# Kernel optimization log

Measured on AMD Instinct MI355X. Metric: run time of the kernel, lower is better.

## Reference

```python
import jax, jax.numpy as jnp
import numpy as np

B, L, D, NC, H = 2, 192, 768, 4, 256  # batch, seq_len, bert_hidden, num_case(+coref), hidden


def setup_inputs() -> dict:
    key = jax.random.key(0)
    ks = jax.random.split(key, 9)
    s = 0.02  # init scale
    return {
        "sequence_output": jax.random.normal(ks[0], (B, L, D), dtype=jnp.float32),
        "base_score": jax.random.normal(ks[1], (B, L, NC, L), dtype=jnp.float32),
        "Wp": jax.random.normal(ks[2], (D, H), dtype=jnp.float32) * s,
        "bp": jnp.zeros((H,), dtype=jnp.float32),
        "Wa": jax.random.normal(ks[3], (D, NC * H), dtype=jnp.float32) * s,
        "ba": jnp.zeros((NC * H,), dtype=jnp.float32),
        "Wmid": jax.random.normal(ks[4], (NC, H + NC, H), dtype=jnp.float32) * s,
        "bmid": jnp.zeros((NC, H), dtype=jnp.float32),
        "Wout": jax.random.normal(ks[5], (NC, H), dtype=jnp.float32) * s,
    }


def reference(sequence_output, base_score, Wp, bp, Wa, ba, Wmid, bmid, Wout):
    b, l, d = sequence_output.shape
    nc = Wmid.shape[0]
    h = Wp.shape[1]
    # dropout is identity in eval mode
    h_p = sequence_output @ Wp + bp                       # [B, L, H] (predicate)
    h_a = (sequence_output @ Wa + ba).reshape(b, l, nc, h)  # [B, L, NC, H] (argument)
    # broadcast add: predicate axis p, argument axis a -> [B, P, A, NC, H]
    h_pa = jnp.tanh(h_p[:, :, None, None, :] + h_a[:, None, :, :, :])
    # base_score [B, L, NC, L] -> transpose(2,3) -> [B, P, A, NC], expand over case axis
    bs = jnp.swapaxes(base_score, 2, 3)                   # [B, P, A, NC]
    bs = jnp.broadcast_to(bs[:, :, :, None, :], (b, l, l, nc, nc))
    hcat = jnp.concatenate([h_pa, bs], axis=-1)           # [B, P, A, NC, H+NC]
    # per-case mid Linear, batched as a single einsum over the case axis n
    h_mid = jnp.tanh(jnp.einsum('bpanc,nch->bpanh', hcat, Wmid) + bmid)
    out = jnp.einsum('bpanh,nh->bpan', h_mid, Wout)       # [B, P, A, NC]
    return jnp.transpose(out, (0, 1, 3, 2))               # [B, P, NC, A]
```

## Files before the change

kernel.cpp:

```cpp
#include <hip/hip_runtime.h>

#define LSEQ 192
#define DIM  768
#define NCASE 4
#define HID  256
#define BATCH 2

#define TANH_K 2.885390081777927f

typedef float  floatx4 __attribute__((ext_vector_type(4)));
typedef __bf16 bf16x8  __attribute__((ext_vector_type(8)));
typedef __bf16 bf16x4  __attribute__((ext_vector_type(4)));

__device__ __forceinline__ float tanh_pre(float x) {
    float e = __builtin_amdgcn_exp2f(x);
    return 1.0f - 2.0f * __builtin_amdgcn_rcpf(e + 1.0f);
}

__device__ __forceinline__ float tanh_add(float tu, float tv) {
    float den = __builtin_fmaf(tu, tv, 1.0f);
    return (tu + tv) * __builtin_amdgcn_rcpf(den);
}

__device__ __forceinline__ void barrier_lds_only() {
    __builtin_amdgcn_sched_barrier(0);
    __builtin_amdgcn_s_waitcnt(0xC07F);
    __builtin_amdgcn_s_barrier();
    __builtin_amdgcn_sched_barrier(0);
}

template <int CTRL>
__device__ __forceinline__ float dpp_add(float v) {
    int x = __builtin_amdgcn_update_dpp(0, __builtin_bit_cast(int, v),
                                        CTRL, 0xF, 0xF, true);
    return v + __builtin_bit_cast(float, x);
}
__device__ __forceinline__ float row16_reduce(float v) {
    v = dpp_add<0xB1>(v);
    v = dpp_add<0x4E>(v);
    v = dpp_add<0x141>(v);
    v = dpp_add<0x140>(v);
    return v;
}


__global__ __launch_bounds__(256) void prep(
    const float* __restrict__ seq, const float* __restrict__ Wp,
    const float* __restrict__ Wa,  const float* __restrict__ bp,
    const float* __restrict__ ba,  const float* __restrict__ Wmid,
    const float* __restrict__ bmid,
    float* __restrict__ lin, bf16x8* __restrict__ Bpack)
{
    const int blk = blockIdx.x;
    const int tid = threadIdx.x;

    if (blk >= 1920) {
        int u = (blk - 1920) * 256 + tid;
        int lane = u & 63, f = u >> 6;
        int ct = f & 15, nk = f >> 4;
        int kc = nk % 9, n = nk / 9;
        int h = ct * 16 + (lane & 15);
        int kbase = kc * 32 + ((lane >> 4) & 3) * 8;
        bf16x8 v;
        #pragma unroll
        for (int j = 0; j < 8; j++) {
            int k = kbase + j;
            float x;
            if (k < 260)       x = Wmid[(size_t)(n * 260 + k) * 256 + h];
            else if (k == 260) x = bmid[n * 256 + h];
            else               x = 0.0f;
            v[j] = (__bf16)(TANH_K * x);
        }
        Bpack[u] = v;
        return;
    }

    const int w = tid >> 6, lane = tid & 63;
    const int rt = blk / 80, cg = blk % 80;
    const int quad  = lane >> 4;
    const int col16 = lane & 15;

    __shared__ float cmb[3][256];

    const int arow = rt * 16 + col16;
    const int col  = cg * 16 + col16;
    const int kofs = w * 192;
    const float* aptr = seq + (size_t)arow * DIM + kofs + quad * 8;
    const float* wbase = (cg < 16) ? (Wp + col) : (Wa + (col - 256));
    const int    wstr  = (cg < 16) ? HID : (NCASE * HID);

    floatx4 acc = {};
    floatx4 a0 = *(const floatx4*)(aptr);
    floatx4 a1 = *(const floatx4*)(aptr + 4);
    float bv[8];
    #pragma unroll
    for (int j = 0; j < 8; j++)
        bv[j] = wbase[(size_t)(kofs + quad * 8 + j) * wstr];

    #pragma unroll
    for (int kc = 0; kc < 6; kc++) {
        bf16x8 ah, al, bh, bl;
        #pragma unroll
        for (int j = 0; j < 4; j++) {
            __bf16 h0 = (__bf16)a0[j];
            ah[j] = h0; al[j] = (__bf16)(a0[j] - (float)h0);
            __bf16 h1 = (__bf16)a1[j];
            ah[4 + j] = h1; al[4 + j] = (__bf16)(a1[j] - (float)h1);
        }
        #pragma unroll
        for (int j = 0; j < 8; j++) {
            __bf16 h = (__bf16)bv[j];
            bh[j] = h; bl[j] = (__bf16)(bv[j] - (float)h);
        }
        if (kc < 5) {
            a0 = *(const floatx4*)(aptr + (kc + 1) * 32);
            a1 = *(const floatx4*)(aptr + (kc + 1) * 32 + 4);
            #pragma unroll
            for (int j = 0; j < 8; j++)
                bv[j] = wbase[(size_t)(kofs + (kc + 1) * 32 + quad * 8 + j) * wstr];
        }
        acc = __builtin_amdgcn_mfma_f32_16x16x32_bf16(ah, bh, acc, 0, 0, 0);
        acc = __builtin_amdgcn_mfma_f32_16x16x32_bf16(al, bh, acc, 0, 0, 0);
        acc = __builtin_amdgcn_mfma_f32_16x16x32_bf16(ah, bl, acc, 0, 0, 0);
    }

    if (w > 0) *(floatx4*)&cmb[w - 1][lane * 4] = acc;
    __syncthreads();
    if (w == 0) {
        #pragma unroll
        for (int i = 0; i < 3; i++) {
            floatx4 p = *(const floatx4*)&cmb[i][lane * 4];
            acc += p;
        }
        const float bias = (cg < 16) ? bp[col] : ba[col - 256];
        #pragma unroll
        for (int reg = 0; reg < 4; reg++)
            lin[(size_t)(rt * 16 + quad * 4 + reg) * 1280 + col] =
                tanh_pre(TANH_K * (acc[reg] + bias));
    }
}

__global__ __launch_bounds__(512, 6) void refine_main(
    const float* __restrict__ lin,
    const float* __restrict__ base_score,
    const float* __restrict__ Wout,
    const bf16x8* __restrict__ Bpack,
    float* __restrict__ out)
{
    const int bx = blockIdx.x;
    const int n  = blockIdx.y;
    const int b  = blockIdx.z;
    const int ptile = bx / 24, atile = bx % 24;
    const int p0 = ptile * 8, a0r = atile * 8;

    const int tid   = threadIdx.x;
    const int w     = tid >> 6;
    const int lane  = tid & 63;
    const int quad  = lane >> 4;
    const int col16 = lane & 15;

    __shared__ __align__(16) __bf16 A0[256 * 8];
    __shared__ __align__(16) __bf16 A1[256 * 8];
    __shared__ float red[8][64];

    const int s_g    = tid >> 1;
    const int h2     = tid & 1;
    const int l_g    = s_g & 63;
    const int m_gen  = ((s_g >> 6) << 4) + (l_g & 15);
    const int kq     = (l_g >> 4) * 8 + h2 * 4;
    const int quad_g = l_g >> 4;

    const int pg = p0 + (m_gen >> 3), ag = a0r + (m_gen & 7);
    const float* hp_ptr = lin + (size_t)(b * LSEQ + pg) * 1280 + kq;
    const float* ha_ptr = lin + (size_t)(b * LSEQ + ag) * 1280 + 256 + n * 256 + kq;

    const bf16x8* bbase = Bpack + ((size_t)(n * 9) * 16 + w * 2) * 64 + lane;

    float bs4[4] = {};
    if (quad_g == 0 && h2 == 0) {
        #pragma unroll
        for (int j = 0; j < 4; j++)
            bs4[j] = base_score[((size_t)(b * LSEQ + pg) * NCASE + j) * LSEQ + ag];
    }
    float wo[2];
    #pragma unroll
    for (int ct = 0; ct < 2; ct++)
        wo[ct] = Wout[n * 256 + w * 32 + ct * 16 + col16];

    bf16x8 bcur[2];
    #pragma unroll
    for (int ct = 0; ct < 2; ct++) bcur[ct] = bbase[ct * 64];

    floatx4 hp = *(const floatx4*)(hp_ptr);
    floatx4 ha = *(const floatx4*)(ha_ptr);
    {
        bf16x4 av;
        #pragma unroll
        for (int j = 0; j < 4; j++) av[j] = (__bf16)tanh_add(hp[j], ha[j]);
        *(bf16x4*)&A0[tid * 4] = av;
    }
    hp = *(const floatx4*)(hp_ptr + 32);
    ha = *(const floatx4*)(ha_ptr + 32);
    barrier_lds_only();

    floatx4 acc[4][2] = {};

    #pragma unroll
    for (int kc = 0; kc < 9; kc++) {
        bf16x8 bnext[2];
        if (kc < 8) {
            #pragma unroll
            for (int ct = 0; ct < 2; ct++)
                bnext[ct] = bbase[((kc + 1) * 16 + ct) * 64];
        }
        if (kc < 7) {
            floatx4 u0 = hp, v0 = ha;
            if (kc < 6) {
                hp = *(const floatx4*)(hp_ptr + (kc + 2) * 32);
                ha = *(const floatx4*)(ha_ptr + (kc + 2) * 32);
            }
            bf16x4 av;
            #pragma unroll
            for (int j = 0; j < 4; j++) av[j] = (__bf16)tanh_add(u0[j], v0[j]);
            __bf16* buf = ((kc + 1) & 1) ? A1 : A0;
            *(bf16x4*)&buf[tid * 4] = av;
        } else if (kc == 7) {
            bf16x4 av = {};
            if (quad_g == 0) {
                if (h2 == 0) {
                    #pragma unroll
                    for (int j = 0; j < 4; j++) av[j] = (__bf16)bs4[j];
                } else {
                    av[0] = (__bf16)1.0f;
                }
            }
            *(bf16x4*)&A0[tid * 4] = av;
        }

        const __bf16* rb = (kc & 1) ? A1 : A0;
        bf16x8 af[4];
        #pragma unroll
        for (int rt = 0; rt < 4; rt++)
            af[rt] = *(const bf16x8*)&rb[(rt * 64 + lane) * 8];
        #pragma unroll
        for (int rt = 0; rt < 4; rt++)
            #pragma unroll
            for (int ct = 0; ct < 2; ct++)
                acc[rt][ct] = __builtin_amdgcn_mfma_f32_16x16x32_bf16(
                    af[rt], bcur[ct], acc[rt][ct], 0, 0, 0);
        #pragma unroll
        for (int ct = 0; ct < 2; ct++) bcur[ct] = bnext[ct];
        if (kc < 8) barrier_lds_only();
    }

    #pragma unroll
    for (int rt = 0; rt < 4; rt++) {
        #pragma unroll
        for (int reg = 0; reg < 4; reg++) {
            float rs = tanh_pre(acc[rt][0][reg]) * wo[0]
                     + tanh_pre(acc[rt][1][reg]) * wo[1];
            rs = row16_reduce(rs);
            if (col16 == 0) red[w][rt * 16 + quad * 4 + reg] = rs;
        }
    }
    barrier_lds_only();

    if (tid < 64) {
        float total = red[0][tid] + red[1][tid] + red[2][tid] + red[3][tid]
                    + red[4][tid] + red[5][tid] + red[6][tid] + red[7][tid];
        const int p = p0 + (tid >> 3), a = a0r + (tid & 7);
        out[((size_t)(b * LSEQ + p) * NCASE + n) * LSEQ + a] = total;
    }
}

extern "C" void kernel_launch(void* const* d_in, const int* in_sizes, int n_in,
                              void* d_out, int out_size, void* d_ws, size_t ws_size,
                              hipStream_t stream) {
    const float* seq  = (const float*)d_in[0];
    const float* bsc  = (const float*)d_in[1];
    const float* Wp   = (const float*)d_in[2];
    const float* bp   = (const float*)d_in[3];
    const float* Wa   = (const float*)d_in[4];
    const float* ba   = (const float*)d_in[5];
    const float* Wmid = (const float*)d_in[6];
    const float* bmid = (const float*)d_in[7];
    const float* Wout = (const float*)d_in[8];
    float* out = (float*)d_out;

    char* ws = (char*)d_ws;
    float*  lin   = (float*)(ws);
    bf16x8* Bpack = (bf16x8*)(ws + 1966080);

    prep<<<2064, 256, 0, stream>>>(seq, Wp, Wa, bp, ba, Wmid, bmid, lin, Bpack);
    refine_main<<<dim3(576, NCASE, BATCH), 512, 0, stream>>>(
        lin, bsc, Wout, Bpack, out);
}
```

Measured before the change: 149.6 us.

## Process two K-chunks per barrier with wider A tiles and packed-float tanh math

The main loop goes from 9 single-chunk stages to 4 double-chunk stages plus a tail. Each thread now builds 8 bf16 values per stage, one half of the threads per chunk, so the number of workgroup barriers is roughly halved. The tanh-add and the final tanh-times-Wout are rewritten with 2-wide float vectors so the compiler can emit packed FMA, add and mul instructions. More B fragments and A data live in registers, so launch_bounds occupancy drops from 6 to 4, and LDS use doubles.

```diff
diff --git a/kernel.cpp b/kernel.cpp
--- a/kernel.cpp
+++ b/kernel.cpp
@@ -9,12 +9,41 @@
 #define TANH_K 2.885390081777927f
 
 typedef float  floatx4 __attribute__((ext_vector_type(4)));
+typedef float  floatx2 __attribute__((ext_vector_type(2)));
 typedef __bf16 bf16x8  __attribute__((ext_vector_type(8)));
 typedef __bf16 bf16x4  __attribute__((ext_vector_type(4)));
 
 __device__ __forceinline__ float tanh_pre(float x) {
     float e = __builtin_amdgcn_exp2f(x);
     return 1.0f - 2.0f * __builtin_amdgcn_rcpf(e + 1.0f);
+}
+
+__device__ __forceinline__ floatx2 pk_fma2(floatx2 a, floatx2 b, floatx2 c) {
+    return __builtin_elementwise_fma(a, b, c);
+}
+__device__ __forceinline__ floatx2 pk_add2(floatx2 a, floatx2 b) { return a + b; }
+__device__ __forceinline__ floatx2 pk_mul2(floatx2 a, floatx2 b) { return a * b; }
+
+__device__ __forceinline__ bf16x8 tanh_add8(floatx4 u0, floatx4 u1,
+                                            floatx4 v0, floatx4 v1) {
+    const floatx2 one = {1.0f, 1.0f};
+    float uu[8] = {u0[0], u0[1], u0[2], u0[3], u1[0], u1[1], u1[2], u1[3]};
+    float vv[8] = {v0[0], v0[1], v0[2], v0[3], v1[0], v1[1], v1[2], v1[3]};
+    bf16x8 r;
+    #pragma unroll
+    for (int i = 0; i < 4; i++) {
+        floatx2 tu = {uu[2 * i], uu[2 * i + 1]};
+        floatx2 tv = {vv[2 * i], vv[2 * i + 1]};
+        floatx2 den = pk_fma2(tu, tv, one);
+        floatx2 num = pk_add2(tu, tv);
+        floatx2 rc;
+        rc[0] = __builtin_amdgcn_rcpf(den[0]);
+        rc[1] = __builtin_amdgcn_rcpf(den[1]);
+        floatx2 res = pk_mul2(num, rc);
+        r[2 * i]     = (__bf16)res[0];
+        r[2 * i + 1] = (__bf16)res[1];
+    }
+    return r;
 }
 
 __device__ __forceinline__ float tanh_add(float tu, float tv) {
@@ -140,7 +169,7 @@
     }
 }
 
-__global__ __launch_bounds__(512, 6) void refine_main(
+__global__ __launch_bounds__(512, 4) void refine_main(
     const float* __restrict__ lin,
     const float* __restrict__ base_score,
     const float* __restrict__ Wout,
@@ -159,25 +188,25 @@
     const int quad  = lane >> 4;
     const int col16 = lane & 15;
 
-    __shared__ __align__(16) __bf16 A0[256 * 8];
-    __shared__ __align__(16) __bf16 A1[256 * 8];
+    __shared__ __align__(16) __bf16 Abuf[2][4096];
     __shared__ float red[8][64];
 
-    const int s_g    = tid >> 1;
-    const int h2     = tid & 1;
-    const int l_g    = s_g & 63;
-    const int m_gen  = ((s_g >> 6) << 4) + (l_g & 15);
-    const int kq     = (l_g >> 4) * 8 + h2 * 4;
-    const int quad_g = l_g >> 4;
+    const int chunk_off = tid >> 8;
+    const int s     = tid & 255;
+    const int m_gen = ((s >> 6) << 4) + (s & 15);
+    const int kq0   = ((s >> 4) & 3) * 8;
 
     const int pg = p0 + (m_gen >> 3), ag = a0r + (m_gen & 7);
-    const float* hp_ptr = lin + (size_t)(b * LSEQ + pg) * 1280 + kq;
-    const float* ha_ptr = lin + (size_t)(b * LSEQ + ag) * 1280 + 256 + n * 256 + kq;
-
-    const bf16x8* bbase = Bpack + ((size_t)(n * 9) * 16 + w * 2) * 64 + lane;
+    const float* hp_b = lin + (size_t)(b * LSEQ + pg) * 1280 + chunk_off * 32 + kq0;
+    const float* ha_b = lin + (size_t)(b * LSEQ + ag) * 1280 + 256 + n * 256
+                        + chunk_off * 32 + kq0;
+
+    const bf16x8* bptr = Bpack + ((size_t)(n * 9) * 16 + w * 2) * 64 + lane;
+
+    __bf16* wptr = &Abuf[0][chunk_off * 2048 + s * 8];
 
     float bs4[4] = {};
-    if (quad_g == 0 && h2 == 0) {
+    if (chunk_off == 0 && kq0 == 0) {
         #pragma unroll
         for (int j = 0; j < 4; j++)
             bs4[j] = base_score[((size_t)(b * LSEQ + pg) * NCASE + j) * LSEQ + ag];
@@ -187,57 +216,79 @@
     for (int ct = 0; ct < 2; ct++)
         wo[ct] = Wout[n * 256 + w * 32 + ct * 16 + col16];
 
-    bf16x8 bcur[2];
-    #pragma unroll
-    for (int ct = 0; ct < 2; ct++) bcur[ct] = bbase[ct * 64];
-
-    floatx4 hp = *(const floatx4*)(hp_ptr);
-    floatx4 ha = *(const floatx4*)(ha_ptr);
+    bf16x8 bfr[2][2][2];
+    #pragma unroll
+    for (int cc = 0; cc < 2; cc++)
+        #pragma unroll
+        for (int ct = 0; ct < 2; ct++)
+            bfr[0][cc][ct] = bptr[(cc * 16 + ct) * 64];
+
+    floatx4 u0 = *(const floatx4*)(hp_b);
+    floatx4 u1 = *(const floatx4*)(hp_b + 4);
+    floatx4 v0 = *(const floatx4*)(ha_b);
+    floatx4 v1 = *(const floatx4*)(ha_b + 4);
+    *(bf16x8*)wptr = tanh_add8(u0, u1, v0, v1);
+    u0 = *(const floatx4*)(hp_b + 64);
+    u1 = *(const floatx4*)(hp_b + 68);
+    v0 = *(const floatx4*)(ha_b + 64);
+    v1 = *(const floatx4*)(ha_b + 68);
+    barrier_lds_only();
+
+    floatx4 acc[4][2] = {};
+
+    #pragma unroll
+    for (int p = 0; p < 4; p++) {
+        if (p < 3) {
+            #pragma unroll
+            for (int cc = 0; cc < 2; cc++)
+                #pragma unroll
+                for (int ct = 0; ct < 2; ct++)
+                    bfr[(p + 1) & 1][cc][ct] =
+                        bptr[((2 * p + 2 + cc) * 16 + ct) * 64];
+        } else {
+            #pragma unroll
+            for (int ct = 0; ct < 2; ct++)
+                bfr[0][0][ct] = bptr[(8 * 16 + ct) * 64];
+        }
+
+        __bf16* wp = wptr + (((p + 1) & 1) ? 4096 : 0);
+        if (p < 3) {
+            *(bf16x8*)wp = tanh_add8(u0, u1, v0, v1);
+            if (p < 2) {
+                u0 = *(const floatx4*)(hp_b + (2 * p + 4) * 32);
+                u1 = *(const floatx4*)(hp_b + (2 * p + 4) * 32 + 4);
+                v0 = *(const floatx4*)(ha_b + (2 * p + 4) * 32);
+                v1 = *(const floatx4*)(ha_b + (2 * p + 4) * 32 + 4);
+            }
+        } else if (chunk_off == 0) {
+            bf16x8 av = {};
+            if (kq0 == 0) {
+                #pragma unroll
+                for (int j = 0; j < 4; j++) av[j] = (__bf16)bs4[j];
+                av[4] = (__bf16)1.0f;
+            }
+            *(bf16x8*)wp = av;
+        }
+
+        #pragma unroll
+        for (int cc = 0; cc < 2; cc++) {
+            const __bf16* rb = &Abuf[p & 1][cc * 2048];
+            bf16x8 af[4];
+            #pragma unroll
+            for (int rt = 0; rt < 4; rt++)
+                af[rt] = *(const bf16x8*)&rb[(rt * 64 + lane) * 8];
+            #pragma unroll
+            for (int rt = 0; rt < 4; rt++)
+                #pragma unroll
+                for (int ct = 0; ct < 2; ct++)
+                    acc[rt][ct] = __builtin_amdgcn_mfma_f32_16x16x32_bf16(
+                        af[rt], bfr[p & 1][cc][ct], acc[rt][ct], 0, 0, 0);
+        }
+        barrier_lds_only();
+    }
+
     {
-        bf16x4 av;
-        #pragma unroll
-        for (int j = 0; j < 4; j++) av[j] = (__bf16)tanh_add(hp[j], ha[j]);
-        *(bf16x4*)&A0[tid * 4] = av;
-    }
-    hp = *(const floatx4*)(hp_ptr + 32);
-    ha = *(const floatx4*)(ha_ptr + 32);
-    barrier_lds_only();
-
-    floatx4 acc[4][2] = {};
-
-    #pragma unroll
-    for (int kc = 0; kc < 9; kc++) {
-        bf16x8 bnext[2];
-        if (kc < 8) {
-            #pragma unroll
-            for (int ct = 0; ct < 2; ct++)
-                bnext[ct] = bbase[((kc + 1) * 16 + ct) * 64];
-        }
-        if (kc < 7) {
-            floatx4 u0 = hp, v0 = ha;
-            if (kc < 6) {
-                hp = *(const floatx4*)(hp_ptr + (kc + 2) * 32);
-                ha = *(const floatx4*)(ha_ptr + (kc + 2) * 32);
-            }
-            bf16x4 av;
-            #pragma unroll
-            for (int j = 0; j < 4; j++) av[j] = (__bf16)tanh_add(u0[j], v0[j]);
-            __bf16* buf = ((kc + 1) & 1) ? A1 : A0;
-            *(bf16x4*)&buf[tid * 4] = av;
-        } else if (kc == 7) {
-            bf16x4 av = {};
-            if (quad_g == 0) {
-                if (h2 == 0) {
-                    #pragma unroll
-                    for (int j = 0; j < 4; j++) av[j] = (__bf16)bs4[j];
-                } else {
-                    av[0] = (__bf16)1.0f;
-                }
-            }
-            *(bf16x4*)&A0[tid * 4] = av;
-        }
-
-        const __bf16* rb = (kc & 1) ? A1 : A0;
+        const __bf16* rb = &Abuf[0][0];
         bf16x8 af[4];
         #pragma unroll
         for (int rt = 0; rt < 4; rt++)
@@ -247,18 +298,24 @@
             #pragma unroll
             for (int ct = 0; ct < 2; ct++)
                 acc[rt][ct] = __builtin_amdgcn_mfma_f32_16x16x32_bf16(
-                    af[rt], bcur[ct], acc[rt][ct], 0, 0, 0);
-        #pragma unroll
-        for (int ct = 0; ct < 2; ct++) bcur[ct] = bnext[ct];
-        if (kc < 8) barrier_lds_only();
-    }
-
+                    af[rt], bfr[0][0][ct], acc[rt][ct], 0, 0, 0);
+    }
+
+    const floatx2 onex2 = {1.0f, 1.0f};
+    const floatx2 m2x2  = {-2.0f, -2.0f};
     #pragma unroll
     for (int rt = 0; rt < 4; rt++) {
         #pragma unroll
         for (int reg = 0; reg < 4; reg++) {
-            float rs = tanh_pre(acc[rt][0][reg]) * wo[0]
-                     + tanh_pre(acc[rt][1][reg]) * wo[1];
+            floatx2 e;
+            e[0] = __builtin_amdgcn_exp2f(acc[rt][0][reg]);
+            e[1] = __builtin_amdgcn_exp2f(acc[rt][1][reg]);
+            floatx2 d = pk_add2(e, onex2);
+            floatx2 rc;
+            rc[0] = __builtin_amdgcn_rcpf(d[0]);
+            rc[1] = __builtin_amdgcn_rcpf(d[1]);
+            floatx2 th = pk_fma2(rc, m2x2, onex2);
+            float rs = __builtin_fmaf(th[1], wo[1], th[0] * wo[0]);
             rs = row16_reduce(rs);
             if (col16 == 0) red[w][rt * 16 + quad * 4 + reg] = rs;
         }
```

Measured after the change: 158.7 us. 6.1% more time.
